# Kernel optimization log

Measured on AMD Instinct MI355X. Metric: run time of the kernel, lower is better.

## Reference

```python
import jax, jax.numpy as jnp
import numpy as np

ALPHA = 15.0
GAMMA = -1.0
STEPS = 20


def setup_inputs() -> dict:
    key = jax.random.key(0)
    k1, k2, k3 = jax.random.split(key, 3)
    V, B, N, D, H = 3, 16, 384, 192, 192
    xs = jax.random.normal(k1, (V, B, N, D), dtype=jnp.float32)
    # normed adjacency: small positive entries so A + A@A stays well scaled
    adjs = jax.random.uniform(k2, (V, B, N, N), dtype=jnp.float32) / N
    W = jax.random.normal(k3, (N, H), dtype=jnp.float32) / np.sqrt(N)
    b = jnp.zeros((H,), dtype=jnp.float32)
    return {"xs": xs, "adjs": adjs, "W": W, "b": b}


def reference(xs, adjs, W, b):
    # xs: [V,B,N,D] per-view node features; adjs: [V,B,N,N] per-view normed adjacency
    V, B, N, D = xs.shape
    alpha, gamma = ALPHA, GAMMA

    # f(A, p=2) = A + A @ A
    a_ls = adjs + jnp.einsum('vbij,vbjk->vbik', adjs, adjs)        # [V,B,N,N]
    # x x^T per view (constant across iterations)
    xxt_v = jnp.einsum('vbnd,vbmd->vbnm', xs, xs)                  # [V,B,N,N]
    xT = jnp.swapaxes(xs, -1, -2)                                  # [V,B,D,N]
    I = jnp.eye(N, dtype=xs.dtype)

    def step(carry, _):
        lambs, _S = carry
        # _update_S
        xxt = jnp.einsum('v,vbnm->bnm', lambs, xxt_v)              # [B,N,N]
        Fasum = jnp.einsum('v,vbnm->bnm', lambs, a_ls)             # [B,N,N]
        Isum = jnp.sum(lambs)
        tmp = jnp.linalg.inv(Isum * alpha * I + xxt)               # [B,N,N]
        S = jnp.einsum('bij,bjk->bik', tmp, alpha * Fasum + xxt)   # [B,N,N]
        # _update_lamb: torch indexes S[j] by view index j (j < B)
        Sv = S[:V]                                                 # [V,N,N]
        recon = xT - jnp.einsum('vbdn,vnm->vbdm', xT, Sv)          # [V,B,D,N]
        e = jnp.sum(recon ** 2, axis=(1, 2, 3)) \
            + alpha * jnp.sum((Sv[:, None] - a_ls) ** 2, axis=(1, 2, 3))
        lambs_new = jnp.power((-1.0 / gamma) * e, 1.0 / (gamma - 1.0))
        return (lambs_new, S), None

    init = (jnp.ones((V,), dtype=xs.dtype), jnp.zeros((B, N, N), dtype=xs.dtype))
    (lambs, S), _ = jax.lax.scan(step, init, None, length=STEPS)

    # MLP(N, nhid): linear projection of the fused structure matrix
    return jnp.einsum('bnm,mh->bnh', S, W) + b
```

## Files before the change

### kernel.cpp

```cpp
#include <hip/hip_runtime.h>
#include <math.h>

#define ALPHA_F 15.0f
constexpr int Nd = 384;
constexpr int Dd = 192;
constexpr int Hd = 192;
constexpr int Vd = 3;
constexpr int Bd = 16;
constexpr long NN  = (long)Nd * Nd;
constexpr long VST = (long)Bd * NN;
constexpr int CB = 128;
constexpr int CB2 = CB * CB;
constexpr long TS = 3 * (long)CB2;


template<bool TA, bool TB, int EPI>
__global__ __launch_bounds__(256) void mm128_kernel(
    const float* __restrict__ A, const float* __restrict__ B,
    float* __restrict__ C, const float* __restrict__ Dp,
    int K, int lda, int ldb, int ldc,
    long sA, long sB, long sC, long sD,
    const float* __restrict__ skipflag)
{
  if (skipflag != nullptr && skipflag[0] != 0.0f) return;
  const int bz = blockIdx.z;
  A += (long)bz * sA; B += (long)bz * sB; C += (long)bz * sC;
  if (EPI == 2) Dp += (long)bz * sD;
  const int tid = threadIdx.x;
  const int row0 = blockIdx.y * 128, col0 = blockIdx.x * 128;
  __shared__ float As[16][132];
  __shared__ float Bs[16][132];
  const int tx = tid & 15, ty = tid >> 4;
  float acc[2][2][4][4] = {};
  for (int k0 = 0; k0 < K; k0 += 16) {
    if (!TA) {
      const int m = tid >> 1, q = (tid & 1) * 8;
      const float* ap = &A[(long)(row0 + m) * lda + k0 + q];
      const float4 a0 = *(const float4*)ap;
      const float4 a1 = *(const float4*)(ap + 4);
      As[q+0][m] = a0.x; As[q+1][m] = a0.y; As[q+2][m] = a0.z; As[q+3][m] = a0.w;
      As[q+4][m] = a1.x; As[q+5][m] = a1.y; As[q+6][m] = a1.z; As[q+7][m] = a1.w;
    } else {
      const int k = tid & 15, m8 = (tid >> 4) * 8;
      const float* ap = &A[(long)(k0 + k) * lda + row0 + m8];
      *(float4*)&As[k][m8]     = *(const float4*)ap;
      *(float4*)&As[k][m8 + 4] = *(const float4*)(ap + 4);
    }
    if (!TB) {
      const int k = tid & 15, n8 = (tid >> 4) * 8;
      const float* bp = &B[(long)(k0 + k) * ldb + col0 + n8];
      *(float4*)&Bs[k][n8]     = *(const float4*)bp;
      *(float4*)&Bs[k][n8 + 4] = *(const float4*)(bp + 4);
    } else {
      const int n = tid >> 1, q = (tid & 1) * 8;
      const float* bp = &B[(long)(col0 + n) * ldb + k0 + q];
      const float4 b0 = *(const float4*)bp;
      const float4 b1 = *(const float4*)(bp + 4);
      Bs[q+0][n] = b0.x; Bs[q+1][n] = b0.y; Bs[q+2][n] = b0.z; Bs[q+3][n] = b0.w;
      Bs[q+4][n] = b1.x; Bs[q+5][n] = b1.y; Bs[q+6][n] = b1.z; Bs[q+7][n] = b1.w;
    }
    __syncthreads();
    #pragma unroll
    for (int kk = 0; kk < 16; ++kk) {
      const float4 a0 = *(const float4*)&As[kk][ty * 4];
      const float4 a1 = *(const float4*)&As[kk][64 + ty * 4];
      const float4 b0 = *(const float4*)&Bs[kk][tx * 4];
      const float4 b1 = *(const float4*)&Bs[kk][64 + tx * 4];
      const float ar[2][4] = {{a0.x,a0.y,a0.z,a0.w},{a1.x,a1.y,a1.z,a1.w}};
      const float br[2][4] = {{b0.x,b0.y,b0.z,b0.w},{b1.x,b1.y,b1.z,b1.w}};
      #pragma unroll
      for (int ra = 0; ra < 2; ++ra)
        #pragma unroll
        for (int r = 0; r < 4; ++r)
          #pragma unroll
          for (int ca = 0; ca < 2; ++ca)
            #pragma unroll
            for (int c = 0; c < 4; ++c)
              acc[ra][ca][r][c] = fmaf(ar[ra][r], br[ca][c], acc[ra][ca][r][c]);
    }
    __syncthreads();
  }
  #pragma unroll
  for (int ra = 0; ra < 2; ++ra)
    #pragma unroll
    for (int r = 0; r < 4; ++r) {
      const int row = row0 + ra * 64 + ty * 4 + r;
      #pragma unroll
      for (int ca = 0; ca < 2; ++ca) {
        const int col = col0 + ca * 64 + tx * 4;
        float4* cp = (float4*)&C[(long)row * ldc + col];
        float4 v = make_float4(acc[ra][ca][r][0], acc[ra][ca][r][1],
                               acc[ra][ca][r][2], acc[ra][ca][r][3]);
        if (EPI == 1) {
          const float4 old = *cp;
          v = make_float4(old.x - v.x, old.y - v.y, old.z - v.z, old.w - v.w);
        } else if (EPI == 2) {
          const float4 d = *(const float4*)&Dp[(long)row * ldc + col];
          v = make_float4(d.x + v.x, d.y + v.y, d.z + v.z, d.w + v.w);
        }
        *cp = v;
      }
    }
}

template<bool TA, bool TB, int EPI>
__global__ __launch_bounds__(256) void mm_kernel(
    const float* __restrict__ A, const float* __restrict__ B,
    float* __restrict__ C, const float* __restrict__ Dp,
    int K, int lda, int ldb, int ldc,
    long sA, long sB, long sC, long sD,
    const float* __restrict__ skipflag)
{
  if (skipflag != nullptr && skipflag[0] != 0.0f) return;
  const int bz = blockIdx.z;
  A += (long)bz * sA;
  B += (long)bz * sB;
  C += (long)bz * sC;
  const int tid = threadIdx.x;
  const int row0 = blockIdx.y * 64, col0 = blockIdx.x * 64;
  __shared__ float As[16][68];
  __shared__ float Bs[16][68];
  const int tx = tid & 15, ty = tid >> 4;
  float acc[4][4] = {};
  for (int k0 = 0; k0 < K; k0 += 16) {
    if (!TA) {
      const int kk = tid & 15, mm = tid >> 4;
      #pragma unroll
      for (int j = 0; j < 4; ++j)
        As[kk][mm + 16*j] = A[(long)(row0 + mm + 16*j) * lda + (k0 + kk)];
    } else {
      const int mm = tid & 63, kq = tid >> 6;
      #pragma unroll
      for (int j = 0; j < 4; ++j)
        As[kq + 4*j][mm] = A[(long)(k0 + kq + 4*j) * lda + (row0 + mm)];
    }
    if (!TB) {
      const int nn = tid & 63, kq = tid >> 6;
      #pragma unroll
      for (int j = 0; j < 4; ++j)
        Bs[kq + 4*j][nn] = B[(long)(k0 + kq + 4*j) * ldb + (col0 + nn)];
    } else {
      const int kk = tid & 15, nn = tid >> 4;
      #pragma unroll
      for (int j = 0; j < 4; ++j)
        Bs[kk][nn + 16*j] = B[(long)(col0 + nn + 16*j) * ldb + (k0 + kk)];
    }
    __syncthreads();
    #pragma unroll
    for (int kk = 0; kk < 16; ++kk) {
      const float4 av = *(const float4*)&As[kk][ty*4];
      const float4 bv = *(const float4*)&Bs[kk][tx*4];
      const float ar[4] = {av.x, av.y, av.z, av.w};
      const float br[4] = {bv.x, bv.y, bv.z, bv.w};
      #pragma unroll
      for (int r = 0; r < 4; ++r)
        #pragma unroll
        for (int c = 0; c < 4; ++c)
          acc[r][c] = fmaf(ar[r], br[c], acc[r][c]);
    }
    __syncthreads();
  }
  #pragma unroll
  for (int r = 0; r < 4; ++r) {
    const int rr = row0 + ty*4 + r;
    #pragma unroll
    for (int c = 0; c < 4; ++c) {
      const int cc = col0 + tx*4 + c;
      const long off = (long)rr * ldc + cc;
      if (EPI == 0)      C[off] = acc[r][c];
      else if (EPI == 1) C[off] -= acc[r][c];
      else               C[off] = acc[r][c] + Dp[cc];
    }
  }
}

constexpr int SW = 48;

__device__ __forceinline__ void solve_mm_acc(
    const float* __restrict__ A, bool trans, int srcRow,
    float (&acc)[4][3], float* Bs, float (*As)[136], int tid)
{
  const int ty = tid >> 4, tx = tid & 15;
  for (int k0 = 0; k0 < 128; k0 += 32) {
    __syncthreads();
    if (!trans) {
      for (int i = tid; i < 1024; i += 512) {
        const int r = i >> 3, f = i & 7;
        const float4 v = *(const float4*)&A[(long)r * 128 + k0 + f * 4];
        As[f*4+0][r] = v.x; As[f*4+1][r] = v.y;
        As[f*4+2][r] = v.z; As[f*4+3][r] = v.w;
      }
    } else {
      for (int i = tid; i < 1024; i += 512) {
        const int k = i >> 5, f = i & 31;
        *(float4*)&As[k][f*4] = *(const float4*)&A[(long)(k0 + k) * 128 + f * 4];
      }
    }
    __syncthreads();
    #pragma unroll 4
    for (int kk = 0; kk < 32; ++kk) {
      float a[4], bv[3];
      #pragma unroll
      for (int i = 0; i < 4; ++i) a[i] = As[kk][ty * 4 + i];
      const float* brow = &Bs[(long)(srcRow + k0 + kk) * SW + tx * 3];
      #pragma unroll
      for (int j = 0; j < 3; ++j) bv[j] = brow[j];
      #pragma unroll
      for (int i = 0; i < 4; ++i)
        #pragma unroll
        for (int j = 0; j < 3; ++j)
          acc[i][j] = fmaf(a[i], bv[j], acc[i][j]);
    }
  }
}

__device__ __forceinline__ void solve_store(
    const float (&acc)[4][3], int dstRow, bool subtract, float* Bs, int tid)
{
  const int ty = tid >> 4, tx = tid & 15;
  __syncthreads();
  #pragma unroll
  for (int i = 0; i < 4; ++i) {
    float* drow = &Bs[(long)(dstRow + ty * 4 + i) * SW + tx * 3];
    #pragma unroll
    for (int j = 0; j < 3; ++j)
      drow[j] = subtract ? (drow[j] - acc[i][j]) : acc[i][j];
  }
}

__global__ __launch_bounds__(512) void solve_kernel(
    const float* __restrict__ Tb, const float* __restrict__ Lp,
    float* __restrict__ M2, const float* __restrict__ skipflag)
{
  if (skipflag != nullptr && skipflag[0] != 0.0f) return;
  const int b = blockIdx.y;
  const int c0 = blockIdx.x * SW;
  const float* T = Tb + (long)b * TS;
  const float* P = Lp + (long)b * TS;
  float* M = M2 + (long)b * NN;
  __shared__ float Bs[384 * SW];
  __shared__ float As[32][136];
  const int tid = threadIdx.x;

  for (int i = tid; i < 384 * (SW / 4); i += 512) {
    const int r = i / (SW / 4), f = i % (SW / 4);
    *(float4*)&Bs[r * SW + f * 4] = *(const float4*)&M[(long)r * Nd + c0 + f * 4];
  }

  float acc[4][3];
  #define ZACC {_Pragma("unroll") for (int i = 0; i < 4; ++i) \
                _Pragma("unroll") for (int j = 0; j < 3; ++j) acc[i][j] = 0.0f;}

  ZACC; solve_mm_acc(T,          false,   0, acc, Bs, As, tid); solve_store(acc,   0, false, Bs, tid);
  ZACC; solve_mm_acc(P,          false,   0, acc, Bs, As, tid); solve_store(acc, 128, true,  Bs, tid);
  ZACC; solve_mm_acc(T + CB2,    false, 128, acc, Bs, As, tid); solve_store(acc, 128, false, Bs, tid);
  ZACC; solve_mm_acc(P + CB2,    false,   0, acc, Bs, As, tid);
        solve_mm_acc(P + 2*CB2,  false, 128, acc, Bs, As, tid); solve_store(acc, 256, true,  Bs, tid);
  ZACC; solve_mm_acc(T + 2*CB2,  false, 256, acc, Bs, As, tid); solve_store(acc, 256, false, Bs, tid);
  ZACC; solve_mm_acc(T + 2*CB2,  true,  256, acc, Bs, As, tid); solve_store(acc, 256, false, Bs, tid);
  ZACC; solve_mm_acc(P + 2*CB2,  true,  256, acc, Bs, As, tid); solve_store(acc, 128, true,  Bs, tid);
  ZACC; solve_mm_acc(T + CB2,    true,  128, acc, Bs, As, tid); solve_store(acc, 128, false, Bs, tid);
  ZACC; solve_mm_acc(P,          true,  128, acc, Bs, As, tid);
        solve_mm_acc(P + CB2,    true,  256, acc, Bs, As, tid); solve_store(acc,   0, true,  Bs, tid);
  ZACC; solve_mm_acc(T,          true,    0, acc, Bs, As, tid); solve_store(acc,   0, false, Bs, tid);
  #undef ZACC

  __syncthreads();
  for (int i = tid; i < 384 * (SW / 4); i += 512) {
    const int r = i / (SW / 4), f = i % (SW / 4);
    *(float4*)&M[(long)r * Nd + c0 + f * 4] = *(const float4*)&Bs[r * SW + f * 4];
  }
}

__global__ __launch_bounds__(256) void build_kernel(
    const float* __restrict__ xxt, const float* __restrict__ als,
    const float* __restrict__ consts, float* __restrict__ M1,
    float* __restrict__ M2, const float* __restrict__ skipflag)
{
  if (skipflag != nullptr && skipflag[0] != 0.0f) return;
  const long idx = (long)blockIdx.x * 256 + threadIdx.x;
  const float l0 = consts[0], l1 = consts[1], l2 = consts[2];
  const float dg = ALPHA_F * (l0 + l1 + l2);
  const int b = (int)(idx / NN);
  const int nm = (int)(idx - (long)b * NN);
  const int n = nm / Nd, m = nm - n * Nd;
  const long o = (long)b * NN + nm;
  const float x0 = xxt[o], x1 = xxt[o + VST], x2 = xxt[o + 2*VST];
  const float a0 = als[o], a1 = als[o + VST], a2 = als[o + 2*VST];
  float m1 = l0*x0 + l1*x1 + l2*x2;
  float m2 = l0*fmaf(ALPHA_F, a0, x0) + l1*fmaf(ALPHA_F, a1, x1)
           + l2*fmaf(ALPHA_F, a2, x2);
  if (n == m) m1 += dg;
  M1[o] = m1;
  M2[o] = m2;
}

__global__ __launch_bounds__(1024) void diag_kernel(
    const float* __restrict__ M1, float* __restrict__ Tb, int k,
    const float* __restrict__ skipflag)
{
  if (skipflag != nullptr && skipflag[0] != 0.0f) return;
  const int b = blockIdx.x;
  const float* A = M1 + (long)b * NN;
  float* T = Tb + (long)b * TS + (long)k * CB2;
  __shared__ float D[128][132];
  __shared__ float W[128][132];
  const int tid = threadIdx.x;
  const int wave = tid >> 6, lane = tid & 63;
  const int o = k * 128;

  for (int i = tid; i < CB2; i += 1024) {
    const int r = i >> 7, c = i & 127;
    const int hi = r > c ? r : c, lo = r > c ? c : r;
    D[r][c] = A[(long)(o + hi) * Nd + o + lo];
  }
  __syncthreads();

  for (int p = 0; p < 8; ++p) {
    const int j0 = p * 16;
    if (wave == 0) {
      float pr[2][16];
      #pragma unroll
      for (int h = 0; h < 2; ++h)
        #pragma unroll
        for (int c = 0; c < 16; ++c)
          pr[h][c] = D[lane + 64*h][j0 + c];
      #pragma unroll
      for (int j = 0; j < 16; ++j) {
        const int jj = j0 + j;
        const float d = __shfl((jj < 64) ? pr[0][j] : pr[1][j], jj & 63);
        const float ljj = sqrtf(d);
        const float linv = 1.0f / ljj;
        #pragma unroll
        for (int h = 0; h < 2; ++h) {
          const int r = lane + 64*h;
          if (r > jj) pr[h][j] *= linv;
          else if (r == jj) pr[h][j] = ljj;
        }
        #pragma unroll
        for (int c = j + 1; c < 16; ++c) {
          const int gc = j0 + c;
          const float w = __shfl((gc < 64) ? pr[0][j] : pr[1][j], gc & 63);
          #pragma unroll
          for (int h = 0; h < 2; ++h) {
            const int r = lane + 64*h;
            if (r > jj) pr[h][c] -= pr[h][j] * w;
          }
        }
      }
      #pragma unroll
      for (int h = 0; h < 2; ++h) {
        const int r = lane + 64*h;
        if (r >= j0)
          #pragma unroll
          for (int c = 0; c < 16; ++c)
            D[r][j0 + c] = pr[h][c];
      }
    }
    __syncthreads();
    const int base = j0 + 16;
    const int R = 128 - base;
    if (R > 0) {
      const int nt = R >> 2;
      const int tot = nt * nt;
      for (int t = tid; t < tot; t += 1024) {
        const int r0 = base + (t / nt) * 4, c0 = base + (t % nt) * 4;
        float accv[4][4] = {};
        #pragma unroll 4
        for (int j = 0; j < 16; ++j) {
          float av[4], bv[4];
          #pragma unroll
          for (int i = 0; i < 4; ++i) { av[i] = D[r0+i][j0+j]; bv[i] = D[c0+i][j0+j]; }
          #pragma unroll
          for (int i = 0; i < 4; ++i)
            #pragma unroll
            for (int j2 = 0; j2 < 4; ++j2)
              accv[i][j2] += av[i] * bv[j2];
        }
        #pragma unroll
        for (int i = 0; i < 4; ++i)
          #pragma unroll
          for (int j2 = 0; j2 < 4; ++j2)
            D[r0+i][c0+j2] -= accv[i][j2];
      }
    }
    __syncthreads();
  }

  for (int i = tid; i < CB2; i += 1024) W[i >> 7][i & 127] = 0.0f;
  __syncthreads();
  if (wave < 8 && lane < 16) {
    const int od = wave * 16, c = lane;
    float t[16];
    #pragma unroll
    for (int r = 0; r < 16; ++r) {
      float s = (r == c) ? 1.0f : 0.0f;
      #pragma unroll
      for (int j = 0; j < r; ++j) s -= D[od + r][od + j] * t[j];
      t[r] = s / D[od + r][od + r];
    }
    #pragma unroll
    for (int r = 0; r < 16; ++r)
      if (r >= c) W[od + r][od + c] = t[r];
  }
  __syncthreads();
  for (int lev = 16; lev <= 64; lev <<= 1) {
    const int npair = 64 / lev;
    const int tot = npair * lev * lev;
    for (int t = tid; t < tot; t += 1024) {
      const int pi = t / (lev * lev);
      const int rr = (t / lev) % lev, cc = t % lev;
      const int op = pi * 2 * lev;
      float s = 0.f;
      for (int j = cc; j < lev; ++j)
        s += D[op + lev + rr][op + j] * W[op + j][op + cc];
      D[rr][64 + pi * lev + cc] = s;
    }
    __syncthreads();
    for (int t = tid; t < tot; t += 1024) {
      const int pi = t / (lev * lev);
      const int rr = (t / lev) % lev, cc = t % lev;
      const int op = pi * 2 * lev;
      float s = 0.f;
      for (int j = 0; j <= rr; ++j)
        s += W[op + lev + rr][op + lev + j] * D[j][64 + pi * lev + cc];
      W[op + lev + rr][op + cc] = -s;
    }
    __syncthreads();
  }
  for (int i = tid; i < CB2; i += 1024)
    T[i] = W[i >> 7][i & 127];
}

__device__ __forceinline__ float wave_red(float s) {
  for (int off = 32; off; off >>= 1) s += __shfl_down(s, off);
  return s;
}

__global__ __launch_bounds__(64) void init_consts_kernel(float* __restrict__ c) {
  const int t = threadIdx.x;
  if (t < 3) c[t] = 1.0f;
  else if (t < 34) c[t] = 0.0f;
}

__global__ __launch_bounds__(256) void reduceGA_kernel(
    const float* __restrict__ xxt, const float* __restrict__ als,
    float* __restrict__ G, float* __restrict__ Av, float* __restrict__ c)
{
  const long idx = (long)blockIdx.x * 256 + threadIdx.x;
  const int v = (int)(idx / NN);
  const long nm = idx - (long)v * NN;
  const int n = (int)(nm / Nd), m = (int)(nm - (long)n * Nd);
  const long base = (long)v * VST + nm;
  float g = 0.f, a = 0.f, a2 = 0.f;
  for (int b = 0; b < Bd; ++b) {
    const float x = xxt[base + (long)b * NN];
    const float t = als[base + (long)b * NN];
    g += x; a += t; a2 += t * t;
  }
  G[idx] = g;
  Av[idx] = a;
  if (n == m) atomicAdd(&c[4 + v], g);
  a2 = wave_red(a2);
  __shared__ float red[4];
  if ((threadIdx.x & 63) == 0) red[threadIdx.x >> 6] = a2;
  __syncthreads();
  if (threadIdx.x == 0)
    atomicAdd(&c[7 + v], red[0] + red[1] + red[2] + red[3]);
}

__global__ __launch_bounds__(256) void gse_kernel(
    const float* __restrict__ G, const float* __restrict__ S,
    const float* __restrict__ Av, float* __restrict__ c,
    const float* __restrict__ skipflag)
{
  if (skipflag != nullptr && skipflag[0] != 0.0f) return;
  const int v = blockIdx.z;
  const float* A = G + (long)v * NN;
  const float* B = S + (long)v * NN;
  const float* Avv = Av + (long)v * NN;
  __shared__ float As[16][68];
  __shared__ float Bs[16][68];
  const int tid = threadIdx.x;
  const int row0 = blockIdx.y * 64, col0 = blockIdx.x * 64;
  const int tx = tid & 15, ty = tid >> 4;
  float acc[4][4] = {};
  for (int k0 = 0; k0 < Nd; k0 += 16) {
    const int kk = tid & 15, mm = tid >> 4;
    #pragma unroll
    for (int j = 0; j < 4; ++j)
      As[kk][mm + 16*j] = A[(long)(row0 + mm + 16*j) * Nd + (k0 + kk)];
    const int nn = tid & 63, kq = tid >> 6;
    #pragma unroll
    for (int j = 0; j < 4; ++j)
      Bs[kq + 4*j][nn] = B[(long)(k0 + kq + 4*j) * Nd + (col0 + nn)];
    __syncthreads();
    #pragma unroll
    for (int kk2 = 0; kk2 < 16; ++kk2) {
      const float4 av4 = *(const float4*)&As[kk2][ty*4];
      const float4 bv4 = *(const float4*)&Bs[kk2][tx*4];
      const float ar[4] = {av4.x, av4.y, av4.z, av4.w};
      const float br[4] = {bv4.x, bv4.y, bv4.z, bv4.w};
      #pragma unroll
      for (int r = 0; r < 4; ++r)
        #pragma unroll
        for (int cc = 0; cc < 4; ++cc)
          acc[r][cc] = fmaf(ar[r], br[cc], acc[r][cc]);
    }
    __syncthreads();
  }
  float s1 = 0.f, s2 = 0.f, s3 = 0.f, s4 = 0.f;
  #pragma unroll
  for (int r = 0; r < 4; ++r) {
    const int rr = row0 + ty*4 + r;
    #pragma unroll
    for (int cc = 0; cc < 4; ++cc) {
      const long off = (long)rr * Nd + col0 + tx*4 + cc;
      const float sv = B[off];
      s2 += acc[r][cc] * sv;
      s1 += A[off] * sv;
      s3 += sv * sv;
      s4 += sv * Avv[off];
    }
  }
  __shared__ float red[4][4];
  s1 = wave_red(s1); s2 = wave_red(s2); s3 = wave_red(s3); s4 = wave_red(s4);
  const int w = tid >> 6;
  if ((tid & 63) == 0) { red[w][0] = s1; red[w][1] = s2; red[w][2] = s3; red[w][3] = s4; }
  __syncthreads();
  if (tid != 0) return;
  {
    float t0 = 0, t1 = 0, t2 = 0, t3 = 0;
    for (int i = 0; i < 4; ++i) { t0 += red[i][0]; t1 += red[i][1]; t2 += red[i][2]; t3 += red[i][3]; }
    atomicAdd(&c[16 + v*4 + 0], t0);
    atomicAdd(&c[16 + v*4 + 1], t1);
    atomicAdd(&c[16 + v*4 + 2], t2);
    atomicAdd(&c[16 + v*4 + 3], t3);
  }
  __threadfence();
  int* ic = (int*)c;
  const int old = atomicAdd(&ic[10], 1);
  if (old != 6 * 6 * 3 - 1) return;

  float a12[12];
  #pragma unroll
  for (int i = 0; i < 12; ++i) a12[i] = atomicAdd(&c[16 + i], 0.0f);
  float lnew[3];
  for (int v2 = 0; v2 < 3; ++v2) {
    const double gS  = a12[v2*4 + 0];
    const double sgs = a12[v2*4 + 1];
    const double ss  = a12[v2*4 + 2];
    const double sa  = a12[v2*4 + 3];
    const double e1 = (double)c[4 + v2] - 2.0 * gS + sgs;
    const double e2 = (double)ALPHA_F * ((double)Bd * ss - 2.0 * sa + (double)c[7 + v2]);
    lnew[v2] = (float)(1.0 / sqrt(e1 + e2));
  }
  const int it = ic[11];
  const int phase = it % 3;
  if (phase == 2) {
    for (int v2 = 0; v2 < 3; ++v2) {
      const float s0 = c[28 + v2], s1h = c[31 + v2];
      const float d1 = s1h - s0, d2 = lnew[v2] - s1h;
      const float den = d2 - d1;
      if (fabsf(den) > 1e-30f) {
        const float la = lnew[v2] - d2 * d2 / den;
        if (la > 0.3f * lnew[v2] && la < 3.0f * lnew[v2]) lnew[v2] = la;
      }
    }
  } else if (phase == 0) {
    c[28] = lnew[0]; c[29] = lnew[1]; c[30] = lnew[2];
  } else {
    c[31] = lnew[0]; c[32] = lnew[1]; c[33] = lnew[2];
  }
  float relmax = 0.0f;
  for (int v2 = 0; v2 < 3; ++v2)
    relmax = fmaxf(relmax, fabsf(lnew[v2] - c[v2]) / fabsf(lnew[v2]));
  c[0] = lnew[0]; c[1] = lnew[1]; c[2] = lnew[2];
  #pragma unroll
  for (int i = 0; i < 12; ++i) c[16 + i] = 0.0f;
  if (relmax < 2e-5f) c[12] = 1.0f;
  ic[11] = it + 1;
  atomicExch(&ic[10], 0);
}

extern "C" void kernel_launch(void* const* d_in, const int* in_sizes, int n_in,
                              void* d_out, int out_size, void* d_ws, size_t ws_size,
                              hipStream_t stream) {
  const float* xs   = (const float*)d_in[0];
  const float* adjs = (const float*)d_in[1];
  const float* W    = (const float*)d_in[2];
  const float* bias = (const float*)d_in[3];
  float* out = (float*)d_out;

  float* ws  = (float*)d_ws;
  float* als = ws;
  float* xxt = als + Vd * VST;
  float* G   = xxt + Vd * VST;
  float* Av  = G + 3 * NN;
  float* M1  = Av + 3 * NN;
  float* M2  = M1 + 16 * NN;
  float* Tb  = M2 + 16 * NN;
  float* Lp  = Tb + 16 * TS;
  float* cst = Lp + 16 * TS;

  init_consts_kernel<<<1, 64, 0, stream>>>(cst);
  mm128_kernel<false, false, 2><<<dim3(3, 3, 48), 256, 0, stream>>>(
      adjs, adjs, als, adjs, Nd, Nd, Nd, Nd, NN, NN, NN, NN, nullptr);
  mm128_kernel<false, true, 0><<<dim3(3, 3, 48), 256, 0, stream>>>(
      xs, xs, xxt, nullptr, Dd, Dd, Dd, Nd,
      (long)Nd * Dd, (long)Nd * Dd, NN, 0, nullptr);
  reduceGA_kernel<<<1728, 256, 0, stream>>>(xxt, als, G, Av, cst);

  for (int s = 0; s < 20; ++s) {
    const int nb = (s == 19) ? 16 : 3;
    const float* fl = (s == 19) ? nullptr : (cst + 12);
    build_kernel<<<nb * 576, 256, 0, stream>>>(xxt, als, cst, M1, M2, fl);

    diag_kernel<<<nb, 1024, 0, stream>>>(M1, Tb, 0, fl);
    mm_kernel<false, true, 0><<<dim3(2, 4, nb), 256, 0, stream>>>(
        M1 + (long)128 * Nd, Tb, Lp, nullptr,
        CB, Nd, CB, CB, NN, TS, TS, 0, fl);
    mm_kernel<false, true, 1><<<dim3(4, 4, nb), 256, 0, stream>>>(
        Lp, Lp, M1 + (long)128 * Nd + 128, nullptr,
        CB, CB, CB, Nd, TS, TS, NN, 0, fl);
    diag_kernel<<<nb, 1024, 0, stream>>>(M1, Tb, 1, fl);
    mm_kernel<false, true, 0><<<dim3(2, 2, nb), 256, 0, stream>>>(
        M1 + (long)256 * Nd + 128, Tb + CB2, Lp + 2 * CB2, nullptr,
        CB, Nd, CB, CB, NN, TS, TS, 0, fl);
    mm_kernel<false, true, 1><<<dim3(2, 2, nb), 256, 0, stream>>>(
        Lp + 2 * CB2, Lp + 2 * CB2, M1 + (long)256 * Nd + 256, nullptr,
        CB, CB, CB, Nd, TS, TS, NN, 0, fl);
    diag_kernel<<<nb, 1024, 0, stream>>>(M1, Tb, 2, fl);

    solve_kernel<<<dim3(Nd / SW, nb), 512, 0, stream>>>(Tb, Lp, M2, fl);

    if (s < 19) {
      gse_kernel<<<dim3(6, 6, 3), 256, 0, stream>>>(G, M2, Av, cst, cst + 12);
    }
  }

  mm_kernel<false, false, 3><<<dim3(3, 6, 16), 256, 0, stream>>>(
      M2, W, out, bias, Nd, Nd, Hd, Hd, NN, 0, (long)Nd * Hd, 0, nullptr);
}
```

Baseline: 1.800 ms.

## Fuse iterative solver loop into one persistent cooperative kernel with grid syncs

Replaces the roughly 200 small per-iteration kernel launches (build, diag, tile GEMMs, solve, gse) with a single cooperative persistent kernel of 128 blocks that uses grid.sync between phases. The lambda update moves to one thread after a grid sync instead of the atomic last-block pattern. The aim is to remove launch overhead and inter-kernel gaps in a latency-bound loop. In exchange the diag and solve phases run on very few blocks while the rest wait at grid barriers, and the GEMM tiles shrink to 64x64 with 512 threads.

```diff
diff --git a/kernel.cpp b/kernel.cpp
--- a/kernel.cpp
+++ b/kernel.cpp
@@ -1,5 +1,8 @@
 #include <hip/hip_runtime.h>
+#include <hip/hip_cooperative_groups.h>
 #include <math.h>
+
+namespace cg = cooperative_groups;
 
 #define ALPHA_F 15.0f
 constexpr int Nd = 384;
@@ -12,6 +15,8 @@
 constexpr int CB = 128;
 constexpr int CB2 = CB * CB;
 constexpr long TS = 3 * (long)CB2;
+constexpr int SW = 48;
+constexpr int GRID = 128;
 
 
 template<bool TA, bool TB, int EPI>
@@ -19,10 +24,8 @@
     const float* __restrict__ A, const float* __restrict__ B,
     float* __restrict__ C, const float* __restrict__ Dp,
     int K, int lda, int ldb, int ldc,
-    long sA, long sB, long sC, long sD,
-    const float* __restrict__ skipflag)
-{
-  if (skipflag != nullptr && skipflag[0] != 0.0f) return;
+    long sA, long sB, long sC, long sD)
+{
   const int bz = blockIdx.z;
   A += (long)bz * sA; B += (long)bz * sB; C += (long)bz * sC;
   if (EPI == 2) Dp += (long)bz * sD;
@@ -91,10 +94,7 @@
         float4* cp = (float4*)&C[(long)row * ldc + col];
         float4 v = make_float4(acc[ra][ca][r][0], acc[ra][ca][r][1],
                                acc[ra][ca][r][2], acc[ra][ca][r][3]);
-        if (EPI == 1) {
-          const float4 old = *cp;
-          v = make_float4(old.x - v.x, old.y - v.y, old.z - v.z, old.w - v.w);
-        } else if (EPI == 2) {
+        if (EPI == 2) {
           const float4 d = *(const float4*)&Dp[(long)row * ldc + col];
           v = make_float4(d.x + v.x, d.y + v.y, d.z + v.z, d.w + v.w);
         }
@@ -103,18 +103,13 @@
     }
 }
 
-template<bool TA, bool TB, int EPI>
-__global__ __launch_bounds__(256) void mm_kernel(
+__global__ __launch_bounds__(256) void mmout_kernel(
     const float* __restrict__ A, const float* __restrict__ B,
     float* __restrict__ C, const float* __restrict__ Dp,
-    int K, int lda, int ldb, int ldc,
-    long sA, long sB, long sC, long sD,
-    const float* __restrict__ skipflag)
-{
-  if (skipflag != nullptr && skipflag[0] != 0.0f) return;
+    int K, int lda, int ldb, int ldc, long sA, long sC)
+{
   const int bz = blockIdx.z;
   A += (long)bz * sA;
-  B += (long)bz * sB;
   C += (long)bz * sC;
   const int tid = threadIdx.x;
   const int row0 = blockIdx.y * 64, col0 = blockIdx.x * 64;
@@ -123,27 +118,17 @@
   const int tx = tid & 15, ty = tid >> 4;
   float acc[4][4] = {};
   for (int k0 = 0; k0 < K; k0 += 16) {
-    if (!TA) {
+    {
       const int kk = tid & 15, mm = tid >> 4;
       #pragma unroll
       for (int j = 0; j < 4; ++j)
         As[kk][mm + 16*j] = A[(long)(row0 + mm + 16*j) * lda + (k0 + kk)];
-    } else {
-      const int mm = tid & 63, kq = tid >> 6;
-      #pragma unroll
-      for (int j = 0; j < 4; ++j)
-        As[kq + 4*j][mm] = A[(long)(k0 + kq + 4*j) * lda + (row0 + mm)];
-    }
-    if (!TB) {
+    }
+    {
       const int nn = tid & 63, kq = tid >> 6;
       #pragma unroll
       for (int j = 0; j < 4; ++j)
         Bs[kq + 4*j][nn] = B[(long)(k0 + kq + 4*j) * ldb + (col0 + nn)];
-    } else {
-      const int kk = tid & 15, nn = tid >> 4;
-      #pragma unroll
-      for (int j = 0; j < 4; ++j)
-        Bs[kk][nn + 16*j] = B[(long)(col0 + nn + 16*j) * ldb + (k0 + kk)];
     }
     __syncthreads();
     #pragma unroll
@@ -166,150 +151,82 @@
     #pragma unroll
     for (int c = 0; c < 4; ++c) {
       const int cc = col0 + tx*4 + c;
-      const long off = (long)rr * ldc + cc;
-      if (EPI == 0)      C[off] = acc[r][c];
-      else if (EPI == 1) C[off] -= acc[r][c];
-      else               C[off] = acc[r][c] + Dp[cc];
-    }
-  }
-}
-
-constexpr int SW = 48;
-
-__device__ __forceinline__ void solve_mm_acc(
-    const float* __restrict__ A, bool trans, int srcRow,
-    float (&acc)[4][3], float* Bs, float (*As)[136], int tid)
-{
-  const int ty = tid >> 4, tx = tid & 15;
-  for (int k0 = 0; k0 < 128; k0 += 32) {
-    __syncthreads();
-    if (!trans) {
-      for (int i = tid; i < 1024; i += 512) {
-        const int r = i >> 3, f = i & 7;
-        const float4 v = *(const float4*)&A[(long)r * 128 + k0 + f * 4];
-        As[f*4+0][r] = v.x; As[f*4+1][r] = v.y;
-        As[f*4+2][r] = v.z; As[f*4+3][r] = v.w;
-      }
-    } else {
-      for (int i = tid; i < 1024; i += 512) {
-        const int k = i >> 5, f = i & 31;
-        *(float4*)&As[k][f*4] = *(const float4*)&A[(long)(k0 + k) * 128 + f * 4];
-      }
-    }
-    __syncthreads();
-    #pragma unroll 4
-    for (int kk = 0; kk < 32; ++kk) {
-      float a[4], bv[3];
-      #pragma unroll
-      for (int i = 0; i < 4; ++i) a[i] = As[kk][ty * 4 + i];
-      const float* brow = &Bs[(long)(srcRow + k0 + kk) * SW + tx * 3];
-      #pragma unroll
-      for (int j = 0; j < 3; ++j) bv[j] = brow[j];
-      #pragma unroll
-      for (int i = 0; i < 4; ++i)
-        #pragma unroll
-        for (int j = 0; j < 3; ++j)
-          acc[i][j] = fmaf(a[i], bv[j], acc[i][j]);
-    }
-  }
-}
-
-__device__ __forceinline__ void solve_store(
-    const float (&acc)[4][3], int dstRow, bool subtract, float* Bs, int tid)
-{
-  const int ty = tid >> 4, tx = tid & 15;
-  __syncthreads();
-  #pragma unroll
-  for (int i = 0; i < 4; ++i) {
-    float* drow = &Bs[(long)(dstRow + ty * 4 + i) * SW + tx * 3];
-    #pragma unroll
-    for (int j = 0; j < 3; ++j)
-      drow[j] = subtract ? (drow[j] - acc[i][j]) : acc[i][j];
-  }
-}
-
-__global__ __launch_bounds__(512) void solve_kernel(
-    const float* __restrict__ Tb, const float* __restrict__ Lp,
-    float* __restrict__ M2, const float* __restrict__ skipflag)
-{
-  if (skipflag != nullptr && skipflag[0] != 0.0f) return;
-  const int b = blockIdx.y;
-  const int c0 = blockIdx.x * SW;
-  const float* T = Tb + (long)b * TS;
-  const float* P = Lp + (long)b * TS;
-  float* M = M2 + (long)b * NN;
-  __shared__ float Bs[384 * SW];
-  __shared__ float As[32][136];
-  const int tid = threadIdx.x;
-
-  for (int i = tid; i < 384 * (SW / 4); i += 512) {
-    const int r = i / (SW / 4), f = i % (SW / 4);
-    *(float4*)&Bs[r * SW + f * 4] = *(const float4*)&M[(long)r * Nd + c0 + f * 4];
-  }
-
-  float acc[4][3];
-  #define ZACC {_Pragma("unroll") for (int i = 0; i < 4; ++i) \
-                _Pragma("unroll") for (int j = 0; j < 3; ++j) acc[i][j] = 0.0f;}
-
-  ZACC; solve_mm_acc(T,          false,   0, acc, Bs, As, tid); solve_store(acc,   0, false, Bs, tid);
-  ZACC; solve_mm_acc(P,          false,   0, acc, Bs, As, tid); solve_store(acc, 128, true,  Bs, tid);
-  ZACC; solve_mm_acc(T + CB2,    false, 128, acc, Bs, As, tid); solve_store(acc, 128, false, Bs, tid);
-  ZACC; solve_mm_acc(P + CB2,    false,   0, acc, Bs, As, tid);
-        solve_mm_acc(P + 2*CB2,  false, 128, acc, Bs, As, tid); solve_store(acc, 256, true,  Bs, tid);
-  ZACC; solve_mm_acc(T + 2*CB2,  false, 256, acc, Bs, As, tid); solve_store(acc, 256, false, Bs, tid);
-  ZACC; solve_mm_acc(T + 2*CB2,  true,  256, acc, Bs, As, tid); solve_store(acc, 256, false, Bs, tid);
-  ZACC; solve_mm_acc(P + 2*CB2,  true,  256, acc, Bs, As, tid); solve_store(acc, 128, true,  Bs, tid);
-  ZACC; solve_mm_acc(T + CB2,    true,  128, acc, Bs, As, tid); solve_store(acc, 128, false, Bs, tid);
-  ZACC; solve_mm_acc(P,          true,  128, acc, Bs, As, tid);
-        solve_mm_acc(P + CB2,    true,  256, acc, Bs, As, tid); solve_store(acc,   0, true,  Bs, tid);
-  ZACC; solve_mm_acc(T,          true,    0, acc, Bs, As, tid); solve_store(acc,   0, false, Bs, tid);
-  #undef ZACC
-
-  __syncthreads();
-  for (int i = tid; i < 384 * (SW / 4); i += 512) {
-    const int r = i / (SW / 4), f = i % (SW / 4);
-    *(float4*)&M[(long)r * Nd + c0 + f * 4] = *(const float4*)&Bs[r * SW + f * 4];
-  }
-}
-
-__global__ __launch_bounds__(256) void build_kernel(
+      C[(long)rr * ldc + cc] = acc[r][c] + Dp[cc];
+    }
+  }
+}
+
+__device__ __forceinline__ float wave_red(float s) {
+  for (int off = 32; off; off >>= 1) s += __shfl_down(s, off);
+  return s;
+}
+
+__global__ __launch_bounds__(64) void init_consts_kernel(float* __restrict__ c) {
+  const int t = threadIdx.x;
+  if (t < 3) c[t] = 1.0f;
+  else if (t < 34) c[t] = 0.0f;
+}
+
+__global__ __launch_bounds__(256) void reduceGA_kernel(
     const float* __restrict__ xxt, const float* __restrict__ als,
-    const float* __restrict__ consts, float* __restrict__ M1,
-    float* __restrict__ M2, const float* __restrict__ skipflag)
-{
-  if (skipflag != nullptr && skipflag[0] != 0.0f) return;
+    float* __restrict__ G, float* __restrict__ Av, float* __restrict__ c)
+{
   const long idx = (long)blockIdx.x * 256 + threadIdx.x;
-  const float l0 = consts[0], l1 = consts[1], l2 = consts[2];
+  const int v = (int)(idx / NN);
+  const long nm = idx - (long)v * NN;
+  const int n = (int)(nm / Nd), m = (int)(nm - (long)n * Nd);
+  const long base = (long)v * VST + nm;
+  float g = 0.f, a = 0.f, a2 = 0.f;
+  for (int b = 0; b < Bd; ++b) {
+    const float x = xxt[base + (long)b * NN];
+    const float t = als[base + (long)b * NN];
+    g += x; a += t; a2 += t * t;
+  }
+  G[idx] = g;
+  Av[idx] = a;
+  if (n == m) atomicAdd(&c[4 + v], g);
+  a2 = wave_red(a2);
+  __shared__ float red[4];
+  if ((threadIdx.x & 63) == 0) red[threadIdx.x >> 6] = a2;
+  __syncthreads();
+  if (threadIdx.x == 0)
+    atomicAdd(&c[7 + v], red[0] + red[1] + red[2] + red[3]);
+}
+
+
+__device__ void phase_build(const float* xxt, const float* als, const float* c,
+                            float* M1, float* M2, int nb, long gtid, long gstride)
+{
+  const float l0 = c[0], l1 = c[1], l2 = c[2];
   const float dg = ALPHA_F * (l0 + l1 + l2);
-  const int b = (int)(idx / NN);
-  const int nm = (int)(idx - (long)b * NN);
-  const int n = nm / Nd, m = nm - n * Nd;
-  const long o = (long)b * NN + nm;
-  const float x0 = xxt[o], x1 = xxt[o + VST], x2 = xxt[o + 2*VST];
-  const float a0 = als[o], a1 = als[o + VST], a2 = als[o + 2*VST];
-  float m1 = l0*x0 + l1*x1 + l2*x2;
-  float m2 = l0*fmaf(ALPHA_F, a0, x0) + l1*fmaf(ALPHA_F, a1, x1)
-           + l2*fmaf(ALPHA_F, a2, x2);
-  if (n == m) m1 += dg;
-  M1[o] = m1;
-  M2[o] = m2;
-}
-
-__global__ __launch_bounds__(1024) void diag_kernel(
-    const float* __restrict__ M1, float* __restrict__ Tb, int k,
-    const float* __restrict__ skipflag)
-{
-  if (skipflag != nullptr && skipflag[0] != 0.0f) return;
-  const int b = blockIdx.x;
+  const long tot = (long)nb * NN;
+  for (long idx = gtid; idx < tot; idx += gstride) {
+    const int b = (int)(idx / NN);
+    const int nm = (int)(idx - (long)b * NN);
+    const int n = nm / Nd, m = nm - n * Nd;
+    const long o = (long)b * NN + nm;
+    const float x0 = xxt[o], x1 = xxt[o + VST], x2 = xxt[o + 2*VST];
+    const float a0 = als[o], a1 = als[o + VST], a2 = als[o + 2*VST];
+    float m1 = l0*x0 + l1*x1 + l2*x2;
+    float m2 = l0*fmaf(ALPHA_F, a0, x0) + l1*fmaf(ALPHA_F, a1, x1)
+             + l2*fmaf(ALPHA_F, a2, x2);
+    if (n == m) m1 += dg;
+    M1[o] = m1;
+    M2[o] = m2;
+  }
+}
+
+__device__ void phase_diag(const float* M1, float* Tb, int k, int b, int tid,
+                           float* sm)
+{
   const float* A = M1 + (long)b * NN;
   float* T = Tb + (long)b * TS + (long)k * CB2;
-  __shared__ float D[128][132];
-  __shared__ float W[128][132];
-  const int tid = threadIdx.x;
+  float (*D)[132] = (float(*)[132])sm;
+  float (*W)[132] = (float(*)[132])(sm + 16896);
   const int wave = tid >> 6, lane = tid & 63;
   const int o = k * 128;
 
-  for (int i = tid; i < CB2; i += 1024) {
+  for (int i = tid; i < CB2; i += 512) {
     const int r = i >> 7, c = i & 127;
     const int hi = r > c ? r : c, lo = r > c ? c : r;
     D[r][c] = A[(long)(o + hi) * Nd + o + lo];
@@ -363,7 +280,7 @@
     if (R > 0) {
       const int nt = R >> 2;
       const int tot = nt * nt;
-      for (int t = tid; t < tot; t += 1024) {
+      for (int t = tid; t < tot; t += 512) {
         const int r0 = base + (t / nt) * 4, c0 = base + (t % nt) * 4;
         float accv[4][4] = {};
         #pragma unroll 4
@@ -387,9 +304,9 @@
     __syncthreads();
   }
 
-  for (int i = tid; i < CB2; i += 1024) W[i >> 7][i & 127] = 0.0f;
-  __syncthreads();
-  if (wave < 8 && lane < 16) {
+  for (int i = tid; i < CB2; i += 512) W[i >> 7][i & 127] = 0.0f;
+  __syncthreads();
+  if (lane < 16) {
     const int od = wave * 16, c = lane;
     float t[16];
     #pragma unroll
@@ -407,7 +324,7 @@
   for (int lev = 16; lev <= 64; lev <<= 1) {
     const int npair = 64 / lev;
     const int tot = npair * lev * lev;
-    for (int t = tid; t < tot; t += 1024) {
+    for (int t = tid; t < tot; t += 512) {
       const int pi = t / (lev * lev);
       const int rr = (t / lev) % lev, cc = t % lev;
       const int op = pi * 2 * lev;
@@ -417,7 +334,7 @@
       D[rr][64 + pi * lev + cc] = s;
     }
     __syncthreads();
-    for (int t = tid; t < tot; t += 1024) {
+    for (int t = tid; t < tot; t += 512) {
       const int pi = t / (lev * lev);
       const int rr = (t / lev) % lev, cc = t % lev;
       const int op = pi * 2 * lev;
@@ -428,143 +345,231 @@
     }
     __syncthreads();
   }
-  for (int i = tid; i < CB2; i += 1024)
+  for (int i = tid; i < CB2; i += 512)
     T[i] = W[i >> 7][i & 127];
-}
-
-__device__ __forceinline__ float wave_red(float s) {
-  for (int off = 32; off; off >>= 1) s += __shfl_down(s, off);
-  return s;
-}
-
-__global__ __launch_bounds__(64) void init_consts_kernel(float* __restrict__ c) {
-  const int t = threadIdx.x;
-  if (t < 3) c[t] = 1.0f;
-  else if (t < 34) c[t] = 0.0f;
-}
-
-__global__ __launch_bounds__(256) void reduceGA_kernel(
-    const float* __restrict__ xxt, const float* __restrict__ als,
-    float* __restrict__ G, float* __restrict__ Av, float* __restrict__ c)
-{
-  const long idx = (long)blockIdx.x * 256 + threadIdx.x;
-  const int v = (int)(idx / NN);
-  const long nm = idx - (long)v * NN;
-  const int n = (int)(nm / Nd), m = (int)(nm - (long)n * Nd);
-  const long base = (long)v * VST + nm;
-  float g = 0.f, a = 0.f, a2 = 0.f;
-  for (int b = 0; b < Bd; ++b) {
-    const float x = xxt[base + (long)b * NN];
-    const float t = als[base + (long)b * NN];
-    g += x; a += t; a2 += t * t;
-  }
-  G[idx] = g;
-  Av[idx] = a;
-  if (n == m) atomicAdd(&c[4 + v], g);
-  a2 = wave_red(a2);
-  __shared__ float red[4];
-  if ((threadIdx.x & 63) == 0) red[threadIdx.x >> 6] = a2;
-  __syncthreads();
-  if (threadIdx.x == 0)
-    atomicAdd(&c[7 + v], red[0] + red[1] + red[2] + red[3]);
-}
-
-__global__ __launch_bounds__(256) void gse_kernel(
-    const float* __restrict__ G, const float* __restrict__ S,
-    const float* __restrict__ Av, float* __restrict__ c,
-    const float* __restrict__ skipflag)
-{
-  if (skipflag != nullptr && skipflag[0] != 0.0f) return;
-  const int v = blockIdx.z;
+  __syncthreads();
+}
+
+__device__ void tile_mm_TB(const float* A, const float* B, float* C,
+                           int lda, int ldb, int ldc, bool sub,
+                           float* sm, int tid)
+{
+  float (*As)[68] = (float(*)[68])sm;
+  float (*Bs)[68] = (float(*)[68])(sm + 16 * 68);
+  const int tx = tid & 15, ty = tid >> 4;
+  float acc[2][4] = {};
+  for (int k0 = 0; k0 < 128; k0 += 16) {
+    {
+      const int k = tid & 15, m = tid >> 4;
+      As[k][m]      = A[(long)m * lda + k0 + k];
+      As[k][m + 32] = A[(long)(m + 32) * lda + k0 + k];
+      Bs[k][m]      = B[(long)m * ldb + k0 + k];
+      Bs[k][m + 32] = B[(long)(m + 32) * ldb + k0 + k];
+    }
+    __syncthreads();
+    #pragma unroll
+    for (int kk = 0; kk < 16; ++kk) {
+      const float a0 = As[kk][ty*2], a1 = As[kk][ty*2 + 1];
+      const float4 bv = *(const float4*)&Bs[kk][tx*4];
+      const float br[4] = {bv.x, bv.y, bv.z, bv.w};
+      #pragma unroll
+      for (int j = 0; j < 4; ++j) {
+        acc[0][j] = fmaf(a0, br[j], acc[0][j]);
+        acc[1][j] = fmaf(a1, br[j], acc[1][j]);
+      }
+    }
+    __syncthreads();
+  }
+  #pragma unroll
+  for (int r = 0; r < 2; ++r) {
+    float* cp = &C[(long)(ty*2 + r) * ldc + tx*4];
+    #pragma unroll
+    for (int j = 0; j < 4; ++j)
+      cp[j] = sub ? (cp[j] - acc[r][j]) : acc[r][j];
+  }
+}
+
+__device__ __forceinline__ void solve_mm_acc(
+    const float* __restrict__ A, bool trans, int srcRow,
+    float (&acc)[4][3], float* Bs, float (*As)[136], int tid)
+{
+  const int ty = tid >> 4, tx = tid & 15;
+  for (int k0 = 0; k0 < 128; k0 += 32) {
+    __syncthreads();
+    if (!trans) {
+      for (int i = tid; i < 1024; i += 512) {
+        const int r = i >> 3, f = i & 7;
+        const float4 v = *(const float4*)&A[(long)r * 128 + k0 + f * 4];
+        As[f*4+0][r] = v.x; As[f*4+1][r] = v.y;
+        As[f*4+2][r] = v.z; As[f*4+3][r] = v.w;
+      }
+    } else {
+      for (int i = tid; i < 1024; i += 512) {
+        const int k = i >> 5, f = i & 31;
+        *(float4*)&As[k][f*4] = *(const float4*)&A[(long)(k0 + k) * 128 + f * 4];
+      }
+    }
+    __syncthreads();
+    #pragma unroll 4
+    for (int kk = 0; kk < 32; ++kk) {
+      float a[4], bv[3];
+      #pragma unroll
+      for (int i = 0; i < 4; ++i) a[i] = As[kk][ty * 4 + i];
+      const float* brow = &Bs[(long)(srcRow + k0 + kk) * SW + tx * 3];
+      #pragma unroll
+      for (int j = 0; j < 3; ++j) bv[j] = brow[j];
+      #pragma unroll
+      for (int i = 0; i < 4; ++i)
+        #pragma unroll
+        for (int j = 0; j < 3; ++j)
+          acc[i][j] = fmaf(a[i], bv[j], acc[i][j]);
+    }
+  }
+}
+
+__device__ __forceinline__ void solve_store(
+    const float (&acc)[4][3], int dstRow, bool subtract, float* Bs, int tid)
+{
+  const int ty = tid >> 4, tx = tid & 15;
+  __syncthreads();
+  #pragma unroll
+  for (int i = 0; i < 4; ++i) {
+    float* drow = &Bs[(long)(dstRow + ty * 4 + i) * SW + tx * 3];
+    #pragma unroll
+    for (int j = 0; j < 3; ++j)
+      drow[j] = subtract ? (drow[j] - acc[i][j]) : acc[i][j];
+  }
+}
+
+__device__ void phase_solve(const float* Tb, const float* Lp, float* M2,
+                            int b, int strip, int tid, float* sm)
+{
+  const int c0 = strip * SW;
+  const float* T = Tb + (long)b * TS;
+  const float* P = Lp + (long)b * TS;
+  float* M = M2 + (long)b * NN;
+  float* Bs = sm;
+  float (*As)[136] = (float(*)[136])(sm + 384 * SW);
+  for (int i = tid; i < 384 * (SW / 4); i += 512) {
+    const int r = i / (SW / 4), f = i % (SW / 4);
+    *(float4*)&Bs[r * SW + f * 4] = *(const float4*)&M[(long)r * Nd + c0 + f * 4];
+  }
+  float acc[4][3];
+  #define ZACC {_Pragma("unroll") for (int i = 0; i < 4; ++i) \
+                _Pragma("unroll") for (int j = 0; j < 3; ++j) acc[i][j] = 0.0f;}
+  ZACC; solve_mm_acc(T,          false,   0, acc, Bs, As, tid); solve_store(acc,   0, false, Bs, tid);
+  ZACC; solve_mm_acc(P,          false,   0, acc, Bs, As, tid); solve_store(acc, 128, true,  Bs, tid);
+  ZACC; solve_mm_acc(T + CB2,    false, 128, acc, Bs, As, tid); solve_store(acc, 128, false, Bs, tid);
+  ZACC; solve_mm_acc(P + CB2,    false,   0, acc, Bs, As, tid);
+        solve_mm_acc(P + 2*CB2,  false, 128, acc, Bs, As, tid); solve_store(acc, 256, true,  Bs, tid);
+  ZACC; solve_mm_acc(T + 2*CB2,  false, 256, acc, Bs, As, tid); solve_store(acc, 256, false, Bs, tid);
+  ZACC; solve_mm_acc(T + 2*CB2,  true,  256, acc, Bs, As, tid); solve_store(acc, 256, false, Bs, tid);
+  ZACC; solve_mm_acc(P + 2*CB2,  true,  256, acc, Bs, As, tid); solve_store(acc, 128, true,  Bs, tid);
+  ZACC; solve_mm_acc(T + CB2,    true,  128, acc, Bs, As, tid); solve_store(acc, 128, false, Bs, tid);
+  ZACC; solve_mm_acc(P,          true,  128, acc, Bs, As, tid);
+        solve_mm_acc(P + CB2,    true,  256, acc, Bs, As, tid); solve_store(acc,   0, true,  Bs, tid);
+  ZACC; solve_mm_acc(T,          true,    0, acc, Bs, As, tid); solve_store(acc,   0, false, Bs, tid);
+  #undef ZACC
+  __syncthreads();
+  for (int i = tid; i < 384 * (SW / 4); i += 512) {
+    const int r = i / (SW / 4), f = i % (SW / 4);
+    *(float4*)&M[(long)r * Nd + c0 + f * 4] = *(const float4*)&Bs[r * SW + f * 4];
+  }
+  __syncthreads();
+}
+
+__device__ void phase_gse(const float* G, const float* S, const float* Av,
+                          float* c, int bid, int tid, float* sm)
+{
+  const int v = bid / 36;
+  const int row0 = ((bid / 6) % 6) * 64, col0 = (bid % 6) * 64;
   const float* A = G + (long)v * NN;
   const float* B = S + (long)v * NN;
   const float* Avv = Av + (long)v * NN;
-  __shared__ float As[16][68];
-  __shared__ float Bs[16][68];
-  const int tid = threadIdx.x;
-  const int row0 = blockIdx.y * 64, col0 = blockIdx.x * 64;
+  float (*As)[68] = (float(*)[68])sm;
+  float (*Bs)[68] = (float(*)[68])(sm + 16 * 68);
   const int tx = tid & 15, ty = tid >> 4;
-  float acc[4][4] = {};
+  float acc[2][4] = {};
   for (int k0 = 0; k0 < Nd; k0 += 16) {
-    const int kk = tid & 15, mm = tid >> 4;
-    #pragma unroll
-    for (int j = 0; j < 4; ++j)
-      As[kk][mm + 16*j] = A[(long)(row0 + mm + 16*j) * Nd + (k0 + kk)];
-    const int nn = tid & 63, kq = tid >> 6;
-    #pragma unroll
-    for (int j = 0; j < 4; ++j)
-      Bs[kq + 4*j][nn] = B[(long)(k0 + kq + 4*j) * Nd + (col0 + nn)];
-    __syncthreads();
-    #pragma unroll
-    for (int kk2 = 0; kk2 < 16; ++kk2) {
-      const float4 av4 = *(const float4*)&As[kk2][ty*4];
-      const float4 bv4 = *(const float4*)&Bs[kk2][tx*4];
-      const float ar[4] = {av4.x, av4.y, av4.z, av4.w};
-      const float br[4] = {bv4.x, bv4.y, bv4.z, bv4.w};
-      #pragma unroll
-      for (int r = 0; r < 4; ++r)
-        #pragma unroll
-        for (int cc = 0; cc < 4; ++cc)
-          acc[r][cc] = fmaf(ar[r], br[cc], acc[r][cc]);
+    {
+      const int k = tid & 15, m = tid >> 4;
+      As[k][m]      = A[(long)(row0 + m) * Nd + k0 + k];
+      As[k][m + 32] = A[(long)(row0 + m + 32) * Nd + k0 + k];
+    }
+    {
+      const int k = tid >> 5, n = (tid & 31) * 2;
+      const float* bp = &B[(long)(k0 + k) * Nd + col0 + n];
+      Bs[k][n]     = bp[0];
+      Bs[k][n + 1] = bp[1];
+    }
+    __syncthreads();
+    #pragma unroll
+    for (int kk = 0; kk < 16; ++kk) {
+      const float a0 = As[kk][ty*2], a1 = As[kk][ty*2 + 1];
+      const float4 bv = *(const float4*)&Bs[kk][tx*4];
+      const float br[4] = {bv.x, bv.y, bv.z, bv.w};
+      #pragma unroll
+      for (int j = 0; j < 4; ++j) {
+        acc[0][j] = fmaf(a0, br[j], acc[0][j]);
+        acc[1][j] = fmaf(a1, br[j], acc[1][j]);
+      }
     }
     __syncthreads();
   }
   float s1 = 0.f, s2 = 0.f, s3 = 0.f, s4 = 0.f;
   #pragma unroll
-  for (int r = 0; r < 4; ++r) {
-    const int rr = row0 + ty*4 + r;
-    #pragma unroll
-    for (int cc = 0; cc < 4; ++cc) {
-      const long off = (long)rr * Nd + col0 + tx*4 + cc;
+  for (int r = 0; r < 2; ++r) {
+    const int rr = row0 + ty*2 + r;
+    #pragma unroll
+    for (int j = 0; j < 4; ++j) {
+      const long off = (long)rr * Nd + col0 + tx*4 + j;
       const float sv = B[off];
-      s2 += acc[r][cc] * sv;
+      s2 += acc[r][j] * sv;
       s1 += A[off] * sv;
       s3 += sv * sv;
       s4 += sv * Avv[off];
     }
   }
-  __shared__ float red[4][4];
   s1 = wave_red(s1); s2 = wave_red(s2); s3 = wave_red(s3); s4 = wave_red(s4);
   const int w = tid >> 6;
-  if ((tid & 63) == 0) { red[w][0] = s1; red[w][1] = s2; red[w][2] = s3; red[w][3] = s4; }
-  __syncthreads();
-  if (tid != 0) return;
-  {
+  if ((tid & 63) == 0) { sm[w*4+0] = s1; sm[w*4+1] = s2; sm[w*4+2] = s3; sm[w*4+3] = s4; }
+  __syncthreads();
+  if (tid == 0) {
     float t0 = 0, t1 = 0, t2 = 0, t3 = 0;
-    for (int i = 0; i < 4; ++i) { t0 += red[i][0]; t1 += red[i][1]; t2 += red[i][2]; t3 += red[i][3]; }
+    for (int i = 0; i < 8; ++i) {
+      t0 += sm[i*4]; t1 += sm[i*4+1]; t2 += sm[i*4+2]; t3 += sm[i*4+3];
+    }
     atomicAdd(&c[16 + v*4 + 0], t0);
     atomicAdd(&c[16 + v*4 + 1], t1);
     atomicAdd(&c[16 + v*4 + 2], t2);
     atomicAdd(&c[16 + v*4 + 3], t3);
   }
-  __threadfence();
+  __syncthreads();
+}
+
+__device__ void lambda_update(float* c)
+{
+  float lnew[3];
+  for (int v = 0; v < 3; ++v) {
+    const double gS  = c[16 + v*4 + 0];
+    const double sgs = c[16 + v*4 + 1];
+    const double ss  = c[16 + v*4 + 2];
+    const double sa  = c[16 + v*4 + 3];
+    const double e1 = (double)c[4 + v] - 2.0 * gS + sgs;
+    const double e2 = (double)ALPHA_F * ((double)Bd * ss - 2.0 * sa + (double)c[7 + v]);
+    lnew[v] = (float)(1.0 / sqrt(e1 + e2));
+  }
   int* ic = (int*)c;
-  const int old = atomicAdd(&ic[10], 1);
-  if (old != 6 * 6 * 3 - 1) return;
-
-  float a12[12];
-  #pragma unroll
-  for (int i = 0; i < 12; ++i) a12[i] = atomicAdd(&c[16 + i], 0.0f);
-  float lnew[3];
-  for (int v2 = 0; v2 < 3; ++v2) {
-    const double gS  = a12[v2*4 + 0];
-    const double sgs = a12[v2*4 + 1];
-    const double ss  = a12[v2*4 + 2];
-    const double sa  = a12[v2*4 + 3];
-    const double e1 = (double)c[4 + v2] - 2.0 * gS + sgs;
-    const double e2 = (double)ALPHA_F * ((double)Bd * ss - 2.0 * sa + (double)c[7 + v2]);
-    lnew[v2] = (float)(1.0 / sqrt(e1 + e2));
-  }
   const int it = ic[11];
   const int phase = it % 3;
   if (phase == 2) {
-    for (int v2 = 0; v2 < 3; ++v2) {
-      const float s0 = c[28 + v2], s1h = c[31 + v2];
-      const float d1 = s1h - s0, d2 = lnew[v2] - s1h;
+    for (int v = 0; v < 3; ++v) {
+      const float s0 = c[28 + v], s1h = c[31 + v];
+      const float d1 = s1h - s0, d2 = lnew[v] - s1h;
       const float den = d2 - d1;
       if (fabsf(den) > 1e-30f) {
-        const float la = lnew[v2] - d2 * d2 / den;
-        if (la > 0.3f * lnew[v2] && la < 3.0f * lnew[v2]) lnew[v2] = la;
+        const float la = lnew[v] - d2 * d2 / den;
+        if (la > 0.3f * lnew[v] && la < 3.0f * lnew[v]) lnew[v] = la;
       }
     }
   } else if (phase == 0) {
@@ -573,14 +578,84 @@
     c[31] = lnew[0]; c[32] = lnew[1]; c[33] = lnew[2];
   }
   float relmax = 0.0f;
-  for (int v2 = 0; v2 < 3; ++v2)
-    relmax = fmaxf(relmax, fabsf(lnew[v2] - c[v2]) / fabsf(lnew[v2]));
+  for (int v = 0; v < 3; ++v)
+    relmax = fmaxf(relmax, fabsf(lnew[v] - c[v]) / fabsf(lnew[v]));
   c[0] = lnew[0]; c[1] = lnew[1]; c[2] = lnew[2];
-  #pragma unroll
   for (int i = 0; i < 12; ++i) c[16 + i] = 0.0f;
   if (relmax < 2e-5f) c[12] = 1.0f;
   ic[11] = it + 1;
-  atomicExch(&ic[10], 0);
+  __threadfence();
+}
+
+__global__ __launch_bounds__(512) void loop_kernel(
+    const float* xxt, const float* als, const float* G, const float* Av,
+    float* M1, float* M2, float* Tb, float* Lp, float* cst)
+{
+  cg::grid_group grid = cg::this_grid();
+  __shared__ float sm[33792];
+  const int bid = blockIdx.x, tid = threadIdx.x;
+  const long gtid = (long)bid * 512 + tid;
+  const long gstride = (long)GRID * 512;
+
+  for (int s = 0; s < 20; ++s) {
+    const bool last = (s == 19);
+    if (!last && *((volatile float*)&cst[12]) != 0.0f) continue;
+    const int nb = last ? 16 : 3;
+
+    phase_build(xxt, als, cst, M1, M2, nb, gtid, gstride);
+    grid.sync();
+
+    if (bid < nb) phase_diag(M1, Tb, 0, bid, tid, sm);
+    grid.sync();
+    for (int t = bid; t < 8 * nb; t += GRID) {
+      const int b = t >> 3, tt = t & 7, tr = tt >> 1, tc = tt & 1;
+      tile_mm_TB(M1 + (long)b*NN + (long)(128 + tr*64)*Nd,
+                 Tb + (long)b*TS + (long)tc*64*128,
+                 Lp + (long)b*TS + (long)tr*64*128 + tc*64,
+                 Nd, 128, 128, false, sm, tid);
+    }
+    grid.sync();
+    for (int t = bid; t < 16 * nb; t += GRID) {
+      const int b = t >> 4, tt = t & 15, tr = tt >> 2, tc = tt & 3;
+      tile_mm_TB(Lp + (long)b*TS + (long)tr*64*128,
+                 Lp + (long)b*TS + (long)tc*64*128,
+                 M1 + (long)b*NN + (long)(128 + tr*64)*Nd + 128 + tc*64,
+                 128, 128, Nd, true, sm, tid);
+    }
+    grid.sync();
+
+    if (bid < nb) phase_diag(M1, Tb, 1, bid, tid, sm);
+    grid.sync();
+    for (int t = bid; t < 4 * nb; t += GRID) {
+      const int b = t >> 2, tt = t & 3, tr = tt >> 1, tc = tt & 1;
+      tile_mm_TB(M1 + (long)b*NN + (long)(256 + tr*64)*Nd + 128,
+                 Tb + (long)b*TS + CB2 + (long)tc*64*128,
+                 Lp + (long)b*TS + 2*CB2 + (long)tr*64*128 + tc*64,
+                 Nd, 128, 128, false, sm, tid);
+    }
+    grid.sync();
+    for (int t = bid; t < 4 * nb; t += GRID) {
+      const int b = t >> 2, tt = t & 3, tr = tt >> 1, tc = tt & 1;
+      tile_mm_TB(Lp + (long)b*TS + 2*CB2 + (long)tr*64*128,
+                 Lp + (long)b*TS + 2*CB2 + (long)tc*64*128,
+                 M1 + (long)b*NN + (long)(256 + tr*64)*Nd + 256 + tc*64,
+                 128, 128, Nd, true, sm, tid);
+    }
+    grid.sync();
+
+    if (bid < nb) phase_diag(M1, Tb, 2, bid, tid, sm);
+    grid.sync();
+
+    if (bid < nb * 8) phase_solve(Tb, Lp, M2, bid >> 3, bid & 7, tid, sm);
+    grid.sync();
+
+    if (!last) {
+      if (bid < 108) phase_gse(G, M2, Av, cst, bid, tid, sm);
+      grid.sync();
+      if (bid == 0 && tid == 0) lambda_update(cst);
+      grid.sync();
+    }
+  }
 }
 
 extern "C" void kernel_launch(void* const* d_in, const int* in_sizes, int n_in,
@@ -605,40 +680,20 @@
 
   init_consts_kernel<<<1, 64, 0, stream>>>(cst);
   mm128_kernel<false, false, 2><<<dim3(3, 3, 48), 256, 0, stream>>>(
-      adjs, adjs, als, adjs, Nd, Nd, Nd, Nd, NN, NN, NN, NN, nullptr);
+      adjs, adjs, als, adjs, Nd, Nd, Nd, Nd, NN, NN, NN, NN);
   mm128_kernel<false, true, 0><<<dim3(3, 3, 48), 256, 0, stream>>>(
       xs, xs, xxt, nullptr, Dd, Dd, Dd, Nd,
-      (long)Nd * Dd, (long)Nd * Dd, NN, 0, nullptr);
+      (long)Nd * Dd, (long)Nd * Dd, NN, 0);
   reduceGA_kernel<<<1728, 256, 0, stream>>>(xxt, als, G, Av, cst);
 
-  for (int s = 0; s < 20; ++s) {
-    const int nb = (s == 19) ? 16 : 3;
-    const float* fl = (s == 19) ? nullptr : (cst + 12);
-    build_kernel<<<nb * 576, 256, 0, stream>>>(xxt, als, cst, M1, M2, fl);
-
-    diag_kernel<<<nb, 1024, 0, stream>>>(M1, Tb, 0, fl);
-    mm_kernel<false, true, 0><<<dim3(2, 4, nb), 256, 0, stream>>>(
-        M1 + (long)128 * Nd, Tb, Lp, nullptr,
-        CB, Nd, CB, CB, NN, TS, TS, 0, fl);
-    mm_kernel<false, true, 1><<<dim3(4, 4, nb), 256, 0, stream>>>(
-        Lp, Lp, M1 + (long)128 * Nd + 128, nullptr,
-        CB, CB, CB, Nd, TS, TS, NN, 0, fl);
-    diag_kernel<<<nb, 1024, 0, stream>>>(M1, Tb, 1, fl);
-    mm_kernel<false, true, 0><<<dim3(2, 2, nb), 256, 0, stream>>>(
-        M1 + (long)256 * Nd + 128, Tb + CB2, Lp + 2 * CB2, nullptr,
-        CB, Nd, CB, CB, NN, TS, TS, 0, fl);
-    mm_kernel<false, true, 1><<<dim3(2, 2, nb), 256, 0, stream>>>(
-        Lp + 2 * CB2, Lp + 2 * CB2, M1 + (long)256 * Nd + 256, nullptr,
-        CB, CB, CB, Nd, TS, TS, NN, 0, fl);
-    diag_kernel<<<nb, 1024, 0, stream>>>(M1, Tb, 2, fl);
-
-    solve_kernel<<<dim3(Nd / SW, nb), 512, 0, stream>>>(Tb, Lp, M2, fl);
-
-    if (s < 19) {
-      gse_kernel<<<dim3(6, 6, 3), 256, 0, stream>>>(G, M2, Av, cst, cst + 12);
-    }
-  }
-
-  mm_kernel<false, false, 3><<<dim3(3, 6, 16), 256, 0, stream>>>(
-      M2, W, out, bias, Nd, Nd, Hd, Hd, NN, 0, (long)Nd * Hd, 0, nullptr);
-}
+  {
+    void* kargs[] = { (void*)&xxt, (void*)&als, (void*)&G, (void*)&Av,
+                      (void*)&M1, (void*)&M2, (void*)&Tb, (void*)&Lp,
+                      (void*)&cst };
+    hipLaunchCooperativeKernel((void*)loop_kernel, dim3(GRID), dim3(512),
+                               kargs, 0, stream);
+  }
+
+  mmout_kernel<<<dim3(3, 6, 16), 256, 0, stream>>>(
+      M2, W, out, bias, Nd, Nd, Hd, Hd, NN, (long)Nd * Hd);
+}
```

Result: slower. 2.102 ms (+16.7%).
